# Kernel tuning notes

Measured on AMD Instinct MI355X. Metric: run time of the kernel, lower is better.

## Reference

```python
import jax, jax.numpy as jnp
import numpy as np

NHEADS = 16  # init kwarg


def setup_inputs() -> dict:
    key = jax.random.key(0)
    ks = jax.random.split(key, 3)
    S, B, E = 2048, 4, 1024
    x = jax.random.normal(ks[0], (S, B, E), dtype=jnp.float32)
    Wqkv = jax.random.normal(ks[1], (E, 3 * E), dtype=jnp.float32) * 0.02
    bqkv = jnp.zeros((3 * E,), dtype=jnp.float32)
    Wout = jax.random.normal(ks[2], (E, E), dtype=jnp.float32) * 0.02
    bout = jnp.zeros((E,), dtype=jnp.float32)
    return {"x": x, "Wqkv": Wqkv, "bqkv": bqkv, "Wout": Wout, "bout": bout}


def reference(x, Wqkv, bqkv, Wout, bout):
    S, B, E = x.shape
    H = NHEADS
    d = E // H
    scale = jnp.sqrt(jnp.asarray(E / H, dtype=x.dtype))  # sqrt(d_head)
    qkv = x @ Wqkv + bqkv                      # (S, B, 3E)
    q, k, v = jnp.split(qkv, 3, axis=-1)       # each (S, B, E)
    # (S, B, E) -> (S, B*H, d) -> (B*H, S, d), matching torch reshape+permute
    q = q.reshape(S, B * H, d).transpose(1, 0, 2)
    k = k.reshape(S, B * H, d).transpose(1, 0, 2)
    v = v.reshape(S, B * H, d).transpose(1, 0, 2)
    scores = jnp.einsum('hsd,htd->hst', q, k) / scale  # (B*H, S, S)
    attn = jax.nn.softmax(scores, axis=-1)
    o = jnp.einsum('hst,htd->hsd', attn, v)    # (B*H, S, d)
    o = o.transpose(1, 0, 2).reshape(S, B, E)  # back to (S, B, E)
    return o @ Wout + bout
```

## Files before the change

kernel.cpp:

```cpp
#include <hip/hip_runtime.h>

typedef short s16x8 __attribute__((ext_vector_type(8)));
typedef float f32x4 __attribute__((ext_vector_type(4)));
typedef float f32x16 __attribute__((ext_vector_type(16)));
typedef unsigned int u32x2 __attribute__((ext_vector_type(2)));
typedef unsigned int u32x4 __attribute__((ext_vector_type(4)));

__device__ inline float bf2f(unsigned short u) {
    union { float f; unsigned int i; } x; x.i = ((unsigned int)u) << 16; return x.f;
}
__device__ inline unsigned short f2bf(float f) {
    union { float f; unsigned int i; } x; x.f = f;
    unsigned int r = x.i + 0x7fff + ((x.i >> 16) & 1);
    return (unsigned short)(r >> 16);
}
__device__ inline unsigned int pack_bf16(float a, float b) {
    unsigned int ia = __float_as_uint(a) + 0x8000u;
    unsigned int ib = __float_as_uint(b) + 0x8000u;
    return __builtin_amdgcn_perm(ib, ia, 0x07060302u);
}

__device__ inline void gload_lds16(const unsigned short* g, unsigned short* l) {
    __builtin_amdgcn_global_load_lds(
        (const __attribute__((address_space(1))) unsigned int*)g,
        (__attribute__((address_space(3))) unsigned int*)l, 16, 0, 0);
}

__global__ void detect_dtype(const unsigned short* __restrict__ x16, int* flag) {
    __shared__ int s[256];
    int tid = threadIdx.x;
    int cnt = 0;
    for (int i = tid; i < 4096; i += 256) {
        unsigned short u = x16[2 * i];
        int e = (u >> 7) & 0xFF;
        if (e >= 117 && e <= 129) cnt++;
    }
    s[tid] = cnt;
    __syncthreads();
    for (int off = 128; off; off >>= 1) {
        if (tid < off) s[tid] += s[tid + off];
        __syncthreads();
    }
    if (tid == 0) *flag = (s[0] < 2048) ? 1 : 0;
}

__global__ void convert_x(const void* __restrict__ in, unsigned short* __restrict__ out,
                          const int* __restrict__ flag, int n) {
    int mode = *flag;
    int i0 = (blockIdx.x * 256 + threadIdx.x) * 8;
    if (i0 >= n) return;
    if (mode) {
        const f32x4* f = (const f32x4*)in;
        f32x4 a = f[i0 >> 2];
        f32x4 c = f[(i0 >> 2) + 1];
        u32x4 o;
        o[0] = pack_bf16(a[0], a[1]);
        o[1] = pack_bf16(a[2], a[3]);
        o[2] = pack_bf16(c[0], c[1]);
        o[3] = pack_bf16(c[2], c[3]);
        *(u32x4*)(out + i0) = o;
    } else {
        *(s16x8*)(out + i0) = *(const s16x8*)((const unsigned short*)in + i0);
    }
}

__global__ void cvt_bias(const void* __restrict__ in, float* __restrict__ out,
                         const int* __restrict__ flag, int n) {
    int i = blockIdx.x * 256 + threadIdx.x;
    if (i >= n) return;
    out[i] = (*flag) ? ((const float*)in)[i] : bf2f(((const unsigned short*)in)[i]);
}

__global__ void transpose_cvt(const void* __restrict__ in, unsigned short* __restrict__ out,
                              const int* __restrict__ flag, int R, int C) {
    __shared__ unsigned short t[64][72];
    int mode = *flag;
    int r0 = blockIdx.y * 64, c0 = blockIdx.x * 64;
    for (int i = threadIdx.x; i < 64 * 64; i += 256) {
        int r = i >> 6, c = i & 63;
        size_t idx = (size_t)(r0 + r) * C + (c0 + c);
        t[r][c] = mode ? f2bf(((const float*)in)[idx]) : ((const unsigned short*)in)[idx];
    }
    __syncthreads();
    for (int i = threadIdx.x; i < 64 * 64; i += 256) {
        int c = i >> 6, r = i & 63;
        out[(size_t)(c0 + c) * R + (r0 + r)] = t[r][c];
    }
}

__global__ __launch_bounds__(256) void transpose_v(
    const unsigned short* __restrict__ qkv, unsigned short* __restrict__ Vt) {
    __shared__ unsigned short t[64][72];
    int bh = blockIdx.y; int b = bh >> 4, h = bh & 15;
    int k0 = blockIdx.x * 64;
    int tid = threadIdx.x;
    int kr = tid >> 2, db = (tid & 3) * 16;
    const unsigned short* src = qkv + ((size_t)(k0 + kr) * 4 + b) * 3072 + 2048 + h * 64 + db;
    *(s16x8*)&t[kr][db] = *(const s16x8*)src;
    *(s16x8*)&t[kr][db + 8] = *(const s16x8*)(src + 8);
    __syncthreads();
    int d = tid >> 2, kb = (tid & 3) * 16;
    unsigned short* dst = Vt + (size_t)bh * 131072 + (size_t)d * 2048 + k0 + kb;
    s16x8 a, c;
#pragma unroll
    for (int j = 0; j < 8; ++j) a[j] = t[kb + j][d];
#pragma unroll
    for (int j = 0; j < 8; ++j) c[j] = t[kb + 8 + j][d];
    *(s16x8*)dst = a;
    *(s16x8*)(dst + 8) = c;
}

__global__ __launch_bounds__(512) void gemm_pipe_kernel(
    const unsigned short* __restrict__ A, const unsigned short* __restrict__ BT,
    const float* __restrict__ bias, void* __restrict__ Cout,
    int M, int N, int K, int qcols, float qscale, const int* __restrict__ outf32flag) {
    __shared__ unsigned short As[3][256 * 64];
    __shared__ unsigned short Bs[3][128 * 64];
    int tid = threadIdx.x;
    int lane = tid & 63, w = tid >> 6;
    int wr = w >> 1, wc = w & 1;
    int g = lane >> 4, qh = lane & 15;
    int m0 = blockIdx.y * 256, n0 = blockIdx.x * 128;
    int vxor = (lane & 7) ^ (lane >> 3);
    int axor = qh & 7;

    f32x4 z = {0.f, 0.f, 0.f, 0.f};
    f32x4 acc[4][4];
#pragma unroll
    for (int m = 0; m < 4; ++m)
#pragma unroll
        for (int n = 0; n < 4; ++n) acc[m][n] = z;

    const unsigned short* Asrc = A + (size_t)(m0 + w * 8 + (lane >> 3)) * K + vxor * 8;
    const unsigned short* Bsrc = BT + (size_t)(n0 + w * 8 + (lane >> 3)) * K + vxor * 8;

#define STAGE_A(buf, t, j) gload_lds16(Asrc + (size_t)(j) * 64 * K + (size_t)(t) * 64, \
                                       &As[buf][0] + (j) * 4096 + w * 512)
#define STAGE_B(buf, t, j) gload_lds16(Bsrc + (size_t)(j) * 64 * K + (size_t)(t) * 64, \
                                       &Bs[buf][0] + (j) * 4096 + w * 512)

    int NT = K >> 6;
    STAGE_A(0, 0, 0); STAGE_A(0, 0, 1); STAGE_A(0, 0, 2); STAGE_A(0, 0, 3);
    STAGE_B(0, 0, 0); STAGE_B(0, 0, 1);
    STAGE_A(1, 1, 0); STAGE_A(1, 1, 1); STAGE_A(1, 1, 2); STAGE_A(1, 1, 3);
    STAGE_B(1, 1, 0); STAGE_B(1, 1, 1);
    asm volatile("s_waitcnt vmcnt(6)" ::: "memory");
    __builtin_amdgcn_s_barrier();

    int cur = 0;
    for (int t = 0; t < NT; ++t) {
        int nx = cur + 2; if (nx >= 3) nx -= 3;
        bool pf = (t + 2) < NT;
        const unsigned short* Ab = &As[cur][0];
        const unsigned short* Bb = &Bs[cur][0];

        s16x8 bf[4][2];
#pragma unroll
        for (int n = 0; n < 4; ++n)
#pragma unroll
            for (int kk = 0; kk < 2; ++kk)
                bf[n][kk] = *(const s16x8*)(Bb + (size_t)(wc * 64 + n * 16 + qh) * 64 +
                                            (((kk * 4 + g) ^ axor) * 8));

        if (pf) { STAGE_A(nx, t + 2, 0); STAGE_A(nx, t + 2, 1); STAGE_B(nx, t + 2, 0); }
        {
            s16x8 af[2][2];
#pragma unroll
            for (int i = 0; i < 2; ++i)
#pragma unroll
                for (int kk = 0; kk < 2; ++kk)
                    af[i][kk] = *(const s16x8*)(Ab + (size_t)(wr * 64 + i * 16 + qh) * 64 +
                                                (((kk * 4 + g) ^ axor) * 8));
            __builtin_amdgcn_s_setprio(1);
#pragma unroll
            for (int kk = 0; kk < 2; ++kk)
#pragma unroll
                for (int i = 0; i < 2; ++i)
#pragma unroll
                    for (int n = 0; n < 4; ++n)
                        acc[i][n] = __builtin_amdgcn_mfma_f32_16x16x32_bf16(af[i][kk], bf[n][kk], acc[i][n], 0, 0, 0);
            __builtin_amdgcn_s_setprio(0);
        }
        __builtin_amdgcn_s_barrier();

        if (pf) { STAGE_A(nx, t + 2, 2); STAGE_A(nx, t + 2, 3); STAGE_B(nx, t + 2, 1); }
        {
            s16x8 af[2][2];
#pragma unroll
            for (int i = 0; i < 2; ++i)
#pragma unroll
                for (int kk = 0; kk < 2; ++kk)
                    af[i][kk] = *(const s16x8*)(Ab + (size_t)(wr * 64 + (i + 2) * 16 + qh) * 64 +
                                                (((kk * 4 + g) ^ axor) * 8));
            __builtin_amdgcn_s_setprio(1);
#pragma unroll
            for (int kk = 0; kk < 2; ++kk)
#pragma unroll
                for (int i = 0; i < 2; ++i)
#pragma unroll
                    for (int n = 0; n < 4; ++n)
                        acc[i + 2][n] = __builtin_amdgcn_mfma_f32_16x16x32_bf16(af[i][kk], bf[n][kk], acc[i + 2][n], 0, 0, 0);
            __builtin_amdgcn_s_setprio(0);
        }
        if (t + 1 < NT) {
            if (pf) asm volatile("s_waitcnt vmcnt(6)" ::: "memory");
            else    asm volatile("s_waitcnt vmcnt(0)" ::: "memory");
            __builtin_amdgcn_s_barrier();
        }
        cur = cur + 1; if (cur >= 3) cur -= 3;
    }
#undef STAGE_A
#undef STAGE_B

    bool f32out = (outf32flag != nullptr) && (*outf32flag != 0);
    int crow0 = m0 + wr * 64;
    int ccol0 = n0 + wc * 64;
#pragma unroll
    for (int n = 0; n < 4; ++n) {
        int col = ccol0 + n * 16 + qh;
        float bv = bias[col];
        float qs = (col < qcols) ? qscale : 1.0f;
#pragma unroll
        for (int m = 0; m < 4; ++m) {
            int rbase = crow0 + m * 16 + g * 4;
#pragma unroll
            for (int qq = 0; qq < 4; ++qq) {
                float v = (acc[m][n][qq] + bv) * qs;
                if (f32out)
                    ((float*)Cout)[(size_t)(rbase + qq) * N + col] = v;
                else
                    ((unsigned short*)Cout)[(size_t)(rbase + qq) * N + col] = f2bf(v);
            }
        }
    }
}

__global__ __launch_bounds__(256) void attn_kernel(
    const unsigned short* __restrict__ qkv, const unsigned short* __restrict__ Vt,
    unsigned short* __restrict__ O) {
    int L = blockIdx.y * 16 + blockIdx.x;
    int xcd = L & 7;
    int i = L >> 3;
    int bh = xcd * 8 + (i & 7);
    int q0 = (i >> 3) << 7;
    int b = bh >> 4, h = bh & 15;
    int tid = threadIdx.x, lane = tid & 63, w = tid >> 6;
    int l31 = lane & 31, l5 = lane >> 5;

    __shared__ unsigned short Ks[8 * 128 * 8];
    __shared__ unsigned short Vs[64 * 16 * 8];

    int qrow = q0 + w * 32 + l31;
    const unsigned short* qp = qkv + ((size_t)qrow * 4 + b) * 3072 + h * 64 + l5 * 8;
    s16x8 qf[4];
#pragma unroll
    for (int st = 0; st < 4; ++st) qf[st] = *(const s16x8*)(qp + st * 16);

    f32x16 z16 = {0.f,0.f,0.f,0.f,0.f,0.f,0.f,0.f,0.f,0.f,0.f,0.f,0.f,0.f,0.f,0.f};
    f32x16 oacc[2];
    oacc[0] = z16; oacc[1] = z16;
    float lrun = 0.f;

    const unsigned short* kbase = qkv + ((size_t)lane * 4 + b) * 3072 + 1024 + h * 64;
    const unsigned short* vbase[4];
#pragma unroll
    for (int j = 0; j < 4; ++j) {
        int id = j * 256 + w * 64 + (tid & 63);
        int d = id >> 4, blk = id & 15;
        vbase[j] = Vt + (size_t)bh * 131072 + (size_t)d * 2048 + ((blk ^ (d & 7)) * 8);
    }

    for (int t = 0; t < 16; ++t) {
        __syncthreads();
#pragma unroll
        for (int j = 0; j < 4; ++j) {
            int gd = w * 2 + (j & 1);
            int khalf = j >> 1;
            gload_lds16(kbase + (size_t)khalf * 786432 + gd * 8,
                        Ks + ((size_t)gd * 128 + khalf * 64) * 8);
        }
#pragma unroll
        for (int j = 0; j < 4; ++j) {
            gload_lds16(vbase[j], Vs + (size_t)(j * 256 + w * 64) * 8);
            vbase[j] += 128;
        }
        kbase += 1572864;
        __syncthreads();

        float rsum = 0.f;
#pragma unroll
        for (int kt = 0; kt < 4; ++kt) {
            f32x16 sc = z16;
#pragma unroll
            for (int st = 0; st < 4; ++st) {
                int gd = st * 2 + l5;
                s16x8 kf = *(const s16x8*)(Ks + ((size_t)gd * 128 + kt * 32 + l31) * 8);
                sc = __builtin_amdgcn_mfma_f32_32x32x16_bf16(kf, qf[st], sc, 0, 0, 0);
            }
            float p[16];
#pragma unroll
            for (int r = 0; r < 16; ++r) {
                p[r] = __builtin_amdgcn_exp2f(sc[r]);
                rsum += p[r];
            }
#pragma unroll
            for (int ks1 = 0; ks1 < 2; ++ks1) {
                unsigned int A0 = pack_bf16(p[8 * ks1 + 0], p[8 * ks1 + 1]);
                unsigned int A1 = pack_bf16(p[8 * ks1 + 2], p[8 * ks1 + 3]);
                unsigned int B0 = pack_bf16(p[8 * ks1 + 4], p[8 * ks1 + 5]);
                unsigned int B1 = pack_bf16(p[8 * ks1 + 6], p[8 * ks1 + 7]);
                u32x2 r0 = __builtin_amdgcn_permlane32_swap(A0, B0, false, false);
                u32x2 r1 = __builtin_amdgcn_permlane32_swap(A1, B1, false, false);
                union { unsigned int u[4]; s16x8 v; } uu;
                uu.u[0] = r0[0];
                uu.u[1] = r1[0];
                uu.u[2] = r0[1];
                uu.u[3] = r1[1];
                int ks = kt * 2 + ks1;
#pragma unroll
                for (int dt = 0; dt < 2; ++dt) {
                    int d = dt * 32 + l31;
                    int kb = (ks * 2 + l5) ^ (d & 7);
                    s16x8 vf = *(const s16x8*)(Vs + ((size_t)d * 16 + kb) * 8);
                    oacc[dt] = __builtin_amdgcn_mfma_f32_32x32x16_bf16(vf, uu.v, oacc[dt], 0, 0, 0);
                }
            }
        }
        rsum += __shfl_xor(rsum, 32);
        lrun += rsum;
    }

    float rl = 1.f / lrun;
    unsigned short* orow = O + ((size_t)qrow * 4 + b) * 1024 + h * 64 + l5 * 4;
#pragma unroll
    for (int dt = 0; dt < 2; ++dt) {
#pragma unroll
        for (int g2 = 0; g2 < 4; ++g2) {
            u32x2 pv;
            pv[0] = pack_bf16(oacc[dt][4 * g2 + 0] * rl, oacc[dt][4 * g2 + 1] * rl);
            pv[1] = pack_bf16(oacc[dt][4 * g2 + 2] * rl, oacc[dt][4 * g2 + 3] * rl);
            *(u32x2*)(orow + dt * 32 + g2 * 8) = pv;
        }
    }
}

extern "C" void kernel_launch(void* const* d_in, const int* in_sizes, int n_in,
                              void* d_out, int out_size, void* d_ws, size_t ws_size,
                              hipStream_t stream) {
    const void* x    = d_in[0];
    const void* Wqkv = d_in[1];
    const void* bqkv = d_in[2];
    const void* Wout = d_in[3];
    const void* bout = d_in[4];

    char* ws = (char*)d_ws;
    unsigned short* qkv   = (unsigned short*)(ws);
    unsigned short* Obuf  = (unsigned short*)(ws + 50331648);
    unsigned short* WqkvT = (unsigned short*)(ws + 67108864);
    unsigned short* WoutT = (unsigned short*)(ws + 73400320);
    unsigned short* xb    = (unsigned short*)(ws + 75497472);
    unsigned short* Vtg   = xb;
    float*          bq_f  = (float*)(ws + 92274688);
    float*          bo_f  = (float*)(ws + 92286976);
    int*            flag  = (int*)(ws + 92291072);

    detect_dtype<<<1, 256, 0, stream>>>((const unsigned short*)x, flag);
    convert_x<<<4096, 256, 0, stream>>>(x, xb, flag, 8388608);
    cvt_bias<<<12, 256, 0, stream>>>(bqkv, bq_f, flag, 3072);
    cvt_bias<<<4, 256, 0, stream>>>(bout, bo_f, flag, 1024);
    transpose_cvt<<<dim3(48, 16), 256, 0, stream>>>(Wqkv, WqkvT, flag, 1024, 3072);
    transpose_cvt<<<dim3(16, 16), 256, 0, stream>>>(Wout, WoutT, flag, 1024, 1024);

    gemm_pipe_kernel<<<dim3(24, 32), 512, 0, stream>>>(xb, WqkvT, bq_f, qkv,
                                                       8192, 3072, 1024, 1024, 0.18033688f, nullptr);
    transpose_v<<<dim3(32, 64), 256, 0, stream>>>(qkv, Vtg);
    attn_kernel<<<dim3(16, 64), 256, 0, stream>>>(qkv, Vtg, Obuf);
    gemm_pipe_kernel<<<dim3(8, 32), 512, 0, stream>>>(Obuf, WoutT, bo_f, d_out,
                                                      8192, 1024, 1024, 0, 1.0f, flag);
}
```

Measured before the change: 271.4 us.

## Fuse dtype detection and input conversions into a single prep kernel

Merges six small prep launches (dtype detection, x conversion, bias conversion, two weight transposes) into one kernel. Every block redoes the dtype check on a smaller sample of 1024 elements, so no separate flag kernel has to run first. It also moves the attention row-sum cross-lane shuffle out of the KV loop so it happens once at the end. This removes launch overhead and serialization, at the cost of redundant detection work in every block and a smaller detection sample.

```diff
diff --git a/kernel.cpp b/kernel.cpp
--- a/kernel.cpp
+++ b/kernel.cpp
@@ -26,12 +26,23 @@
         (__attribute__((address_space(3))) unsigned int*)l, 16, 0, 0);
 }
 
-__global__ void detect_dtype(const unsigned short* __restrict__ x16, int* flag) {
+__global__ __launch_bounds__(256) void prep_kernel(
+    const void* __restrict__ x, const void* __restrict__ Wqkv,
+    const void* __restrict__ bqkv, const void* __restrict__ Wout,
+    const void* __restrict__ bout,
+    unsigned short* __restrict__ xb, unsigned short* __restrict__ WqkvT,
+    unsigned short* __restrict__ WoutT, float* __restrict__ bq_f,
+    float* __restrict__ bo_f, int* __restrict__ flag) {
     __shared__ int s[256];
+    __shared__ unsigned short t[64][72];
     int tid = threadIdx.x;
+    int bid = blockIdx.x;
+
+    const unsigned short* x16 = (const unsigned short*)x;
     int cnt = 0;
-    for (int i = tid; i < 4096; i += 256) {
-        unsigned short u = x16[2 * i];
+#pragma unroll
+    for (int k = 0; k < 4; ++k) {
+        unsigned short u = x16[2 * (tid * 4 + k)];
         int e = (u >> 7) & 0xFF;
         if (e >= 117 && e <= 129) cnt++;
     }
@@ -41,51 +52,60 @@
         if (tid < off) s[tid] += s[tid + off];
         __syncthreads();
     }
-    if (tid == 0) *flag = (s[0] < 2048) ? 1 : 0;
-}
-
-__global__ void convert_x(const void* __restrict__ in, unsigned short* __restrict__ out,
-                          const int* __restrict__ flag, int n) {
-    int mode = *flag;
-    int i0 = (blockIdx.x * 256 + threadIdx.x) * 8;
-    if (i0 >= n) return;
-    if (mode) {
-        const f32x4* f = (const f32x4*)in;
-        f32x4 a = f[i0 >> 2];
-        f32x4 c = f[(i0 >> 2) + 1];
-        u32x4 o;
-        o[0] = pack_bf16(a[0], a[1]);
-        o[1] = pack_bf16(a[2], a[3]);
-        o[2] = pack_bf16(c[0], c[1]);
-        o[3] = pack_bf16(c[2], c[3]);
-        *(u32x4*)(out + i0) = o;
-    } else {
-        *(s16x8*)(out + i0) = *(const s16x8*)((const unsigned short*)in + i0);
-    }
-}
-
-__global__ void cvt_bias(const void* __restrict__ in, float* __restrict__ out,
-                         const int* __restrict__ flag, int n) {
-    int i = blockIdx.x * 256 + threadIdx.x;
-    if (i >= n) return;
-    out[i] = (*flag) ? ((const float*)in)[i] : bf2f(((const unsigned short*)in)[i]);
-}
-
-__global__ void transpose_cvt(const void* __restrict__ in, unsigned short* __restrict__ out,
-                              const int* __restrict__ flag, int R, int C) {
-    __shared__ unsigned short t[64][72];
-    int mode = *flag;
-    int r0 = blockIdx.y * 64, c0 = blockIdx.x * 64;
-    for (int i = threadIdx.x; i < 64 * 64; i += 256) {
-        int r = i >> 6, c = i & 63;
-        size_t idx = (size_t)(r0 + r) * C + (c0 + c);
-        t[r][c] = mode ? f2bf(((const float*)in)[idx]) : ((const unsigned short*)in)[idx];
-    }
-    __syncthreads();
-    for (int i = threadIdx.x; i < 64 * 64; i += 256) {
-        int c = i >> 6, r = i & 63;
-        out[(size_t)(c0 + c) * R + (r0 + r)] = t[r][c];
-    }
+    int mode = (s[0] < 512) ? 1 : 0;
+
+    if (bid < 4096) {
+        int i0 = bid * 2048 + tid * 8;
+        if (mode) {
+            const f32x4* f = (const f32x4*)x;
+            f32x4 a = f[i0 >> 2];
+            f32x4 c = f[(i0 >> 2) + 1];
+            u32x4 o;
+            o[0] = pack_bf16(a[0], a[1]);
+            o[1] = pack_bf16(a[2], a[3]);
+            o[2] = pack_bf16(c[0], c[1]);
+            o[3] = pack_bf16(c[2], c[3]);
+            *(u32x4*)(xb + i0) = o;
+        } else {
+            *(s16x8*)(xb + i0) = *(const s16x8*)((const unsigned short*)x + i0);
+        }
+        return;
+    }
+    if (bid < 5120) {
+        const void* in;
+        unsigned short* out;
+        int R = 1024, C, bx, by;
+        if (bid < 4864) {
+            in = Wqkv; out = WqkvT; C = 3072;
+            int b2 = bid - 4096; bx = b2 % 48; by = b2 / 48;
+        } else {
+            in = Wout; out = WoutT; C = 1024;
+            int b2 = bid - 4864; bx = b2 % 16; by = b2 / 16;
+        }
+        int r0 = by * 64, c0 = bx * 64;
+        for (int i = tid; i < 64 * 64; i += 256) {
+            int r = i >> 6, c = i & 63;
+            size_t idx = (size_t)(r0 + r) * C + (c0 + c);
+            t[r][c] = mode ? f2bf(((const float*)in)[idx]) : ((const unsigned short*)in)[idx];
+        }
+        __syncthreads();
+        for (int i = tid; i < 64 * 64; i += 256) {
+            int c = i >> 6, r = i & 63;
+            out[(size_t)(c0 + c) * R + (r0 + r)] = t[r][c];
+        }
+        return;
+    }
+    if (bid < 5136) {
+        int i = (bid - 5120) * 256 + tid;
+        if (i < 3072)
+            bq_f[i] = mode ? ((const float*)bqkv)[i] : bf2f(((const unsigned short*)bqkv)[i]);
+        else {
+            int j = i - 3072;
+            bo_f[j] = mode ? ((const float*)bout)[j] : bf2f(((const unsigned short*)bout)[j]);
+        }
+        return;
+    }
+    if (tid == 0) *flag = mode;
 }
 
 __global__ __launch_bounds__(256) void transpose_v(
@@ -287,7 +307,6 @@
         kbase += 1572864;
         __syncthreads();
 
-        float rsum = 0.f;
 #pragma unroll
         for (int kt = 0; kt < 4; ++kt) {
             f32x16 sc = z16;
@@ -301,7 +320,7 @@
 #pragma unroll
             for (int r = 0; r < 16; ++r) {
                 p[r] = __builtin_amdgcn_exp2f(sc[r]);
-                rsum += p[r];
+                lrun += p[r];
             }
 #pragma unroll
             for (int ks1 = 0; ks1 < 2; ++ks1) {
@@ -326,9 +345,9 @@
                 }
             }
         }
-        rsum += __shfl_xor(rsum, 32);
-        lrun += rsum;
-    }
+    }
+
+    lrun += __shfl_xor(lrun, 32);
 
     float rl = 1.f / lrun;
     unsigned short* orow = O + ((size_t)qrow * 4 + b) * 1024 + h * 64 + l5 * 4;
@@ -364,12 +383,8 @@
     float*          bo_f  = (float*)(ws + 92286976);
     int*            flag  = (int*)(ws + 92291072);
 
-    detect_dtype<<<1, 256, 0, stream>>>((const unsigned short*)x, flag);
-    convert_x<<<4096, 256, 0, stream>>>(x, xb, flag, 8388608);
-    cvt_bias<<<12, 256, 0, stream>>>(bqkv, bq_f, flag, 3072);
-    cvt_bias<<<4, 256, 0, stream>>>(bout, bo_f, flag, 1024);
-    transpose_cvt<<<dim3(48, 16), 256, 0, stream>>>(Wqkv, WqkvT, flag, 1024, 3072);
-    transpose_cvt<<<dim3(16, 16), 256, 0, stream>>>(Wout, WoutT, flag, 1024, 1024);
+    prep_kernel<<<5137, 256, 0, stream>>>(x, Wqkv, bqkv, Wout, bout,
+                                          xb, WqkvT, WoutT, bq_f, bo_f, flag);
 
     gemm_pipe_kernel<<<dim3(24, 32), 512, 0, stream>>>(xb, WqkvT, bq_f, qkv,
                                                        8192, 3072, 1024, 1024, 0.18033688f, nullptr);
```

Measured after the change: 257.5 us. 5.1% less time.
